# Performance work log

Measured on AMD Instinct MI355X. Metric: run time of the kernel, lower is better.

Reference implementation:

```python
import jax, jax.numpy as jnp
import numpy as np

NUM_CLASSES = 21
EPS = 1e-06


def setup_inputs() -> dict:
    key = jax.random.key(0)
    k1, k2 = jax.random.split(key)
    predictions = jax.random.normal(k1, (16, NUM_CLASSES, 512, 512), dtype=jnp.float32)
    targets = jax.random.randint(k2, (16, 512, 512), 0, NUM_CLASSES, dtype=jnp.int32)
    return {"predictions": predictions, "targets": targets}


def reference(predictions, targets):
    C = NUM_CLASSES
    # argmax over channel dim -> [B, H, W] predicted class ids
    pred = jnp.argmax(predictions, axis=1).ravel()
    tgt = targets.ravel().astype(pred.dtype)
    ones = jnp.ones_like(pred, dtype=jnp.float32)
    # single-pass histogram counts (the fused form of the per-class loop)
    pred_cnt = jnp.zeros((C,), jnp.float32).at[pred].add(ones)
    tgt_cnt = jnp.zeros((C,), jnp.float32).at[tgt].add(ones)
    # intersection: count positions where pred == tgt == c; route mismatches to bin C
    inter_idx = jnp.where(pred == tgt, pred, C)
    inter = jnp.zeros((C + 1,), jnp.float32).at[inter_idx].add(ones)[:C]
    union = pred_cnt + tgt_cnt - inter  # == count((pred_mask + tgt_mask) > 0)
    iou = jnp.where(union > 0, inter / (union + EPS), 0.0)
    return jnp.mean(iou)
```

## Files before the change

kernel.cpp:

```cpp
#include <hip/hip_runtime.h>

#define C    21
#define HW4  65536

typedef float f4 __attribute__((ext_vector_type(4)));
typedef int   i4 __attribute__((ext_vector_type(4)));

__global__ __launch_bounds__(256, 4) void iou_hist_kernel(
    const f4* __restrict__ pred4, const i4* __restrict__ tgt4,
    unsigned int* __restrict__ hist) {
  __shared__ unsigned int sh[3 * C];
  const int tid = threadIdx.x;
  if (tid < 3 * C) sh[tid] = 0;
  __syncthreads();

  const int lane = tid & 63;
  const int wv   = tid >> 6;
  const int bid  = blockIdx.x;
  const int b    = bid >> 6;
  const int win  = (bid & 63) << 10;
  const int goff = win + (wv << 8) + lane;
  const int base0 = ((b * C) << 16) + goff;

  f4 best[4]; i4 idx[4];
#pragma unroll
  for (int j = 0; j < 4; ++j) {
    best[j] = pred4[base0 + (j << 6)];
    idx[j]  = (i4)0;
  }
#pragma unroll
  for (int cc = 1; cc < C; cc += 2) {
    f4 v[2][4];
#pragma unroll
    for (int k = 0; k < 2; ++k)
#pragma unroll
      for (int j = 0; j < 4; ++j)
        v[k][j] = pred4[base0 + ((cc + k) << 16) + (j << 6)];
#pragma unroll
    for (int k = 0; k < 2; ++k)
#pragma unroll
      for (int j = 0; j < 4; ++j)
#pragma unroll
        for (int e = 0; e < 4; ++e)
          if (v[k][j][e] > best[j][e]) { best[j][e] = v[k][j][e]; idx[j][e] = cc + k; }
  }

  i4 tg[4];
#pragma unroll
  for (int j = 0; j < 4; ++j) tg[j] = tgt4[(b << 16) + goff + (j << 6)];

  unsigned long long m[16];
#pragma unroll
  for (int j = 0; j < 4; ++j)
#pragma unroll
    for (int e = 0; e < 4; ++e)
      m[j * 4 + e] = __ballot(idx[j][e] == tg[j][e]);

  unsigned int cp = 0, ct = 0, ci = 0;
#pragma unroll
  for (int c = 0; c < C; ++c) {
    unsigned int np_ = 0, nt_ = 0, ni_ = 0;
#pragma unroll
    for (int j = 0; j < 4; ++j)
#pragma unroll
      for (int e = 0; e < 4; ++e) {
        const unsigned long long pb = __ballot(idx[j][e] == c);
        np_ += (unsigned)__popcll(pb);
        ni_ += (unsigned)__popcll(pb & m[j * 4 + e]);
        nt_ += (unsigned)__popcll(__ballot(tg[j][e] == c));
      }
    if (lane == c) { cp = np_; ct = nt_; ci = ni_; }
  }

  if (lane < C) {
    atomicAdd(&sh[lane], cp);
    atomicAdd(&sh[C + lane], ct);
    atomicAdd(&sh[2 * C + lane], ci);
  }
  __syncthreads();
  if (tid < 3 * C) atomicAdd(&hist[tid], sh[tid]);
}

__global__ __launch_bounds__(64) void iou_finalize_kernel(
    const unsigned int* __restrict__ hist, float* __restrict__ out) {
  const int lane = threadIdx.x;
  float iou = 0.0f;
  if (lane < C) {
    const float p = (float)hist[lane];
    const float t = (float)hist[C + lane];
    const float i = (float)hist[2 * C + lane];
    const float u = p + t - i;
    iou = (u > 0.0f) ? (i / (u + 1e-6f)) : 0.0f;
  }
#pragma unroll
  for (int off = 32; off > 0; off >>= 1) iou += __shfl_down(iou, off);
  if (lane == 0) out[0] = iou / (float)C;
}

extern "C" void kernel_launch(void* const* d_in, const int* in_sizes, int n_in,
                              void* d_out, int out_size, void* d_ws, size_t ws_size,
                              hipStream_t stream) {
  const f4* pred = (const f4*)d_in[0];
  const i4* tgt  = (const i4*)d_in[1];
  float*    out  = (float*)d_out;
  unsigned int* hist = (unsigned int*)d_ws;

  hipMemsetAsync(d_ws, 0, 3 * C * sizeof(unsigned int), stream);

  iou_hist_kernel<<<1024, 256, 0, stream>>>(pred, tgt, hist);
  iou_finalize_kernel<<<1, 64, 0, stream>>>(hist, out);
}
```

Before: 119.9 us.

## Fuse finalize into histogram kernel via last-block ticket and regrid work

Merges the finalize kernel into the histogram kernel. A global atomic ticket picks the last block, which computes the mean IoU, so one launch is removed. Work is redistributed over 2048 blocks with 2 groups per thread, and up to 7 channel loads are issued per batch, trading per-thread work for more in-flight loads and blocks. Each block adds a threadfence and a ticket atomic, and the launch-bounds occupancy hint is dropped.

```diff
diff --git a/kernel.cpp b/kernel.cpp
--- a/kernel.cpp
+++ b/kernel.cpp
@@ -1,73 +1,77 @@
 #include <hip/hip_runtime.h>
 
-#define C    21
-#define HW4  65536
+#define C      21
+#define HW4    65536
+#define NGRP   1048576
+#define NBLK   2048
+#define GPT    2
+#define TICKET 63
 
 typedef float f4 __attribute__((ext_vector_type(4)));
 typedef int   i4 __attribute__((ext_vector_type(4)));
 
-__global__ __launch_bounds__(256, 4) void iou_hist_kernel(
-    const f4* __restrict__ pred4, const i4* __restrict__ tgt4,
-    unsigned int* __restrict__ hist) {
+__global__ __launch_bounds__(256) void iou_kernel(
+    const f4* __restrict__ pred, const i4* __restrict__ tgt,
+    unsigned int* __restrict__ hist, float* __restrict__ out) {
   __shared__ unsigned int sh[3 * C];
-  const int tid = threadIdx.x;
+  __shared__ int sh_last;
+  const int tid  = threadIdx.x;
   if (tid < 3 * C) sh[tid] = 0;
   __syncthreads();
+  const int lane = tid & 63;
 
-  const int lane = tid & 63;
-  const int wv   = tid >> 6;
-  const int bid  = blockIdx.x;
-  const int b    = bid >> 6;
-  const int win  = (bid & 63) << 10;
-  const int goff = win + (wv << 8) + lane;
-  const int base0 = ((b * C) << 16) + goff;
+  int idx[GPT][4];
+  i4  tg[GPT];
 
-  f4 best[4]; i4 idx[4];
 #pragma unroll
-  for (int j = 0; j < 4; ++j) {
-    best[j] = pred4[base0 + (j << 6)];
-    idx[j]  = (i4)0;
-  }
+  for (int q = 0; q < GPT; ++q) {
+    const int g    = blockIdx.x * 256 + tid + q * (NBLK * 256);
+    const int b    = g >> 16;
+    const int hw4  = g & (HW4 - 1);
+    const int base = ((b * C) << 16) + hw4;
+
+    f4 best = pred[base];
+    int i0 = 0, i1 = 0, i2 = 0, i3 = 0;
+
 #pragma unroll
-  for (int cc = 1; cc < C; cc += 2) {
-    f4 v[2][4];
+    for (int cc = 1; cc < C; cc += 7) {
+      f4 v[7];
 #pragma unroll
-    for (int k = 0; k < 2; ++k)
+      for (int j = 0; j < 7; ++j)
+        if (cc + j < C) v[j] = pred[base + ((cc + j) << 16)];
 #pragma unroll
-      for (int j = 0; j < 4; ++j)
-        v[k][j] = pred4[base0 + ((cc + k) << 16) + (j << 6)];
-#pragma unroll
-    for (int k = 0; k < 2; ++k)
-#pragma unroll
-      for (int j = 0; j < 4; ++j)
-#pragma unroll
-        for (int e = 0; e < 4; ++e)
-          if (v[k][j][e] > best[j][e]) { best[j][e] = v[k][j][e]; idx[j][e] = cc + k; }
+      for (int j = 0; j < 7; ++j)
+        if (cc + j < C) {
+          const int c = cc + j;
+          if (v[j][0] > best[0]) { best[0] = v[j][0]; i0 = c; }
+          if (v[j][1] > best[1]) { best[1] = v[j][1]; i1 = c; }
+          if (v[j][2] > best[2]) { best[2] = v[j][2]; i2 = c; }
+          if (v[j][3] > best[3]) { best[3] = v[j][3]; i3 = c; }
+        }
+    }
+    idx[q][0] = i0; idx[q][1] = i1; idx[q][2] = i2; idx[q][3] = i3;
+    tg[q] = tgt[g];
   }
 
-  i4 tg[4];
+  unsigned long long m[GPT][4];
 #pragma unroll
-  for (int j = 0; j < 4; ++j) tg[j] = tgt4[(b << 16) + goff + (j << 6)];
-
-  unsigned long long m[16];
-#pragma unroll
-  for (int j = 0; j < 4; ++j)
+  for (int q = 0; q < GPT; ++q)
 #pragma unroll
     for (int e = 0; e < 4; ++e)
-      m[j * 4 + e] = __ballot(idx[j][e] == tg[j][e]);
+      m[q][e] = __ballot(idx[q][e] == tg[q][e]);
 
   unsigned int cp = 0, ct = 0, ci = 0;
 #pragma unroll
   for (int c = 0; c < C; ++c) {
     unsigned int np_ = 0, nt_ = 0, ni_ = 0;
 #pragma unroll
-    for (int j = 0; j < 4; ++j)
+    for (int q = 0; q < GPT; ++q)
 #pragma unroll
       for (int e = 0; e < 4; ++e) {
-        const unsigned long long pb = __ballot(idx[j][e] == c);
+        const unsigned long long pb = __ballot(idx[q][e] == c);
         np_ += (unsigned)__popcll(pb);
-        ni_ += (unsigned)__popcll(pb & m[j * 4 + e]);
-        nt_ += (unsigned)__popcll(__ballot(tg[j][e] == c));
+        ni_ += (unsigned)__popcll(pb & m[q][e]);
+        nt_ += (unsigned)__popcll(__ballot(tg[q][e] == c));
       }
     if (lane == c) { cp = np_; ct = nt_; ci = ni_; }
   }
@@ -79,22 +83,27 @@
   }
   __syncthreads();
   if (tid < 3 * C) atomicAdd(&hist[tid], sh[tid]);
-}
 
-__global__ __launch_bounds__(64) void iou_finalize_kernel(
-    const unsigned int* __restrict__ hist, float* __restrict__ out) {
-  const int lane = threadIdx.x;
-  float iou = 0.0f;
-  if (lane < C) {
-    const float p = (float)hist[lane];
-    const float t = (float)hist[C + lane];
-    const float i = (float)hist[2 * C + lane];
-    const float u = p + t - i;
-    iou = (u > 0.0f) ? (i / (u + 1e-6f)) : 0.0f;
+  __threadfence();
+  __syncthreads();
+  if (tid == 0) {
+    const unsigned int o = atomicAdd(&hist[TICKET], 1u);
+    sh_last = (o == NBLK - 1);
   }
+  __syncthreads();
+  if (sh_last && tid < 64) {
+    float iou = 0.0f;
+    if (tid < C) {
+      const float p = (float)atomicAdd(&hist[tid], 0u);
+      const float t = (float)atomicAdd(&hist[C + tid], 0u);
+      const float i = (float)atomicAdd(&hist[2 * C + tid], 0u);
+      const float u = p + t - i;
+      iou = (u > 0.0f) ? (i / (u + 1e-6f)) : 0.0f;
+    }
 #pragma unroll
-  for (int off = 32; off > 0; off >>= 1) iou += __shfl_down(iou, off);
-  if (lane == 0) out[0] = iou / (float)C;
+    for (int off = 32; off > 0; off >>= 1) iou += __shfl_down(iou, off);
+    if (tid == 0) out[0] = iou / (float)C;
+  }
 }
 
 extern "C" void kernel_launch(void* const* d_in, const int* in_sizes, int n_in,
@@ -105,8 +114,7 @@
   float*    out  = (float*)d_out;
   unsigned int* hist = (unsigned int*)d_ws;
 
-  hipMemsetAsync(d_ws, 0, 3 * C * sizeof(unsigned int), stream);
+  hipMemsetAsync(d_ws, 0, 64 * sizeof(unsigned int), stream);
 
-  iou_hist_kernel<<<1024, 256, 0, stream>>>(pred, tgt, hist);
-  iou_finalize_kernel<<<1, 64, 0, stream>>>(hist, out);
+  iou_kernel<<<NBLK, 256, 0, stream>>>(pred, tgt, hist, out);
 }
```

Result: slower. 381.5 us (+218.1%).
